# Optimization experiments

Measured on AMD Instinct MI355X. Metric: run time of the kernel, lower is better.

The kernel has to match this reference:

```python
import jax, jax.numpy as jnp
import numpy as np

B, S, HID = 2, 2048, 2048
NH, NKV, HD = 16, 4, 128
EPS = 1e-6
THETA = 10000.0
NEG = jnp.float32(-1e30)


def setup_inputs() -> dict:
    key = jax.random.key(0)
    ks = jax.random.split(key, 7)
    return {
        "hidden_states": jax.random.normal(ks[0], (B, S, HID), jnp.float32) * 0.02,
        "positions": jnp.broadcast_to(jnp.arange(S, dtype=jnp.int32), (B, S)),
        "Wq": jax.random.normal(ks[1], (HID, NH * HD), jnp.float32) * (HID ** -0.5),
        "Wk": jax.random.normal(ks[2], (HID, NKV * HD), jnp.float32) * (HID ** -0.5),
        "Wv": jax.random.normal(ks[3], (HID, NKV * HD), jnp.float32) * (HID ** -0.5),
        "Wc": jax.random.normal(ks[4], (NH * HD, HID), jnp.float32) * ((NH * HD) ** -0.5),
        "q_scale": jax.random.uniform(ks[5], (HD,), jnp.float32),
        "k_scale": jax.random.uniform(ks[6], (HD,), jnp.float32),
    }


def _rmsnorm(x, scale):
    # per-head RMSNorm over head_dim (nnx.RMSNorm semantics)
    return x * jax.lax.rsqrt(jnp.mean(x * x, axis=-1, keepdims=True) + EPS) * scale


def _rope_neox(x, positions):
    # x: [B, S, H, HD]; full rotary_dim == HD, neox style (split halves)
    half = HD // 2
    inv_freq = 1.0 / (THETA ** (jnp.arange(half, dtype=jnp.float32) / half))
    ang = positions[..., None].astype(jnp.float32) * inv_freq  # [B, S, half]
    cos = jnp.cos(ang)[:, :, None, :]
    sin = jnp.sin(ang)[:, :, None, :]
    x1, x2 = jnp.split(x, 2, axis=-1)
    return jnp.concatenate([x1 * cos - x2 * sin, x2 * cos + x1 * sin], axis=-1)


def reference(hidden_states, positions, Wq, Wk, Wv, Wc, q_scale, k_scale):
    q = (hidden_states @ Wq).reshape(B, S, NH, HD)
    k = (hidden_states @ Wk).reshape(B, S, NKV, HD)
    v = (hidden_states @ Wv).reshape(B, S, NKV, HD)
    q = _rmsnorm(q, q_scale)
    k = _rmsnorm(k, k_scale)
    q = _rope_neox(q, positions)
    k = _rope_neox(k, positions)
    # GQA: expand KV heads to query heads
    rep = NH // NKV
    k = jnp.repeat(k, rep, axis=2)
    v = jnp.repeat(v, rep, axis=2)
    scores = jnp.einsum("bqhd,bkhd->bhqk", q, k) * (HD ** -0.5)
    causal = jnp.tril(jnp.ones((S, S), dtype=bool))
    scores = jnp.where(causal, scores, NEG)
    probs = jax.nn.softmax(scores, axis=-1)
    attn = jnp.einsum("bhqk,bkhd->bqhd", probs, v).reshape(B, S, NH * HD)
    return attn @ Wc
```

## Files before the change

### kernel.cpp

```cpp
#include <hip/hip_runtime.h>
#include <stdint.h>

typedef unsigned short u16;
typedef unsigned int u32;
typedef __bf16 bf16x8 __attribute__((ext_vector_type(8)));
typedef float f32x4 __attribute__((ext_vector_type(4)));
typedef u32 u32x4 __attribute__((ext_vector_type(4)));

__device__ __forceinline__ u16 f2bf(float x){
  u32 u = __float_as_uint(x);
  u += 0x7FFFu + ((u >> 16) & 1u);
  return (u16)(u >> 16);
}
__device__ __forceinline__ float bf2f(u16 h){
  return __uint_as_float(((u32)h) << 16);
}
__device__ __forceinline__ u32 cvt_pk_bf16(float lo, float hi){
  u32 r;
  asm("v_cvt_pk_bf16_f32 %0, %1, %2" : "=v"(r) : "v"(lo), "v"(hi));
  return r;
}
__device__ __forceinline__ f32x4 mfma16(bf16x8 a, bf16x8 b, f32x4 c){
  return __builtin_amdgcn_mfma_f32_16x16x32_bf16(a, b, c, 0, 0, 0);
}
__device__ __forceinline__ void gload16(const void* g, const void* l){
  __builtin_amdgcn_global_load_lds(
      (__attribute__((address_space(1))) void*)(uintptr_t)g,
      (__attribute__((address_space(3))) void*)(u32)(uintptr_t)l,
      16, 0, 0);
}

__global__ __launch_bounds__(256) void k_prep(const float* __restrict__ hidden,
    const float* __restrict__ Wq, const float* __restrict__ Wk, const float* __restrict__ Wv,
    const float* __restrict__ Wc, u16* __restrict__ hid_bf, u16* __restrict__ wqkv_t,
    u16* __restrict__ wct, float* __restrict__ ct, float* __restrict__ st){
  __shared__ float tile[32][33];
  int bid = blockIdx.x;
  int t = threadIdx.x;
  if (bid < 8192){
    int i = (bid * 256 + t) * 4;
    float4 v = *(const float4*)(hidden + i);
    ushort4 o;
    o.x = f2bf(v.x); o.y = f2bf(v.y); o.z = f2bf(v.z); o.w = f2bf(v.w);
    *(ushort4*)(hid_bf + i) = o;
    return;
  }
  if (bid < 8192 + 6144){
    int b2 = bid - 8192;
    int nb = (b2 % 96) * 32, kb = (b2 / 96) * 32;
    int tx = t & 31, ty = t >> 5;
    #pragma unroll
    for (int j = 0; j < 4; j++){
      int k = kb + ty + j*8;
      int n = nb + tx;
      float v;
      if (n < 2048)      v = Wq[(size_t)k*2048 + n];
      else if (n < 2560) v = Wk[(size_t)k*512 + (n - 2048)];
      else               v = Wv[(size_t)k*512 + (n - 2560)];
      tile[tx][ty + j*8] = v;
    }
    __syncthreads();
    #pragma unroll
    for (int j = 0; j < 4; j++){
      int n = nb + ty + j*8;
      wqkv_t[(size_t)n*2048 + kb + tx] = f2bf(tile[ty + j*8][tx]);
    }
    return;
  }
  if (bid < 8192 + 6144 + 4096){
    int b3 = bid - 8192 - 6144;
    int nb = (b3 % 64) * 32, kb = (b3 / 64) * 32;
    int tx = t & 31, ty = t >> 5;
    #pragma unroll
    for (int j = 0; j < 4; j++){
      tile[tx][ty + j*8] = Wc[(size_t)(kb + ty + j*8)*2048 + nb + tx];
    }
    __syncthreads();
    #pragma unroll
    for (int j = 0; j < 4; j++){
      wct[(size_t)(nb + ty + j*8)*2048 + kb + tx] = f2bf(tile[ty + j*8][tx]);
    }
    return;
  }
  {
    int b4 = bid - 8192 - 6144 - 4096;
    int idx = b4 * 256 + t;
    int p = idx >> 6, i = idx & 63;
    float freq = powf(10000.0f, -(float)i / 64.0f);
    float ang = (float)p * freq;
    ct[idx] = cosf(ang);
    st[idx] = sinf(ang);
  }
}

__global__ __launch_bounds__(256) void k_gemm_qkv(const u16* __restrict__ A, const u16* __restrict__ Bt,
    u16* __restrict__ qkv, u16* __restrict__ vt, int K){
  __shared__ u16 lds[16384];
  int tid = threadIdx.x;
  int lane = tid & 63, w = tid >> 6;
  int g = lane >> 4, c16 = lane & 15;
  int wr = w >> 1, wc = w & 1;
  int chunk = gridDim.x >> 3;
  int logical = (blockIdx.x & 7) * chunk + (blockIdx.x >> 3);
  int bx = logical % 24, by = logical / 24;
  size_t bm = (size_t)by * 128, bn = (size_t)bx * 128;
  f32x4 zero = {0.f, 0.f, 0.f, 0.f};
  f32x4 acc[4][4];
  #pragma unroll
  for (int i=0;i<4;i++)
    #pragma unroll
    for (int j=0;j<4;j++) acc[i][j] = zero;

  int jj = (w*2)*64 + lane;
  const int nt = K >> 5;
  #pragma unroll
  for (int p = 0; p < 2; p++){
    int j = jj + p*64;
    int r = j >> 2, slot = j & 3;
    gload16(A  + (bm + r)*(size_t)K + slot*8, (const char*)(lds)        + (w*2+p)*1024);
    gload16(Bt + (bn + r)*(size_t)K + slot*8, (const char*)(lds + 8192) + (w*2+p)*1024);
  }
  asm volatile("s_waitcnt vmcnt(0)" ::: "memory");
  __builtin_amdgcn_s_barrier();

  int cur = 0;
  #pragma unroll 1
  for (int t = 0; t < nt; ++t){
    if (t + 1 < nt){
      int k0 = (t + 1) << 5;
      #pragma unroll
      for (int p = 0; p < 2; p++){
        int j = jj + p*64;
        int r = j >> 2, slot = j & 3;
        gload16(A  + (bm + r)*(size_t)K + k0 + slot*8, (const char*)(lds + (cur^1)*4096)        + (w*2+p)*1024);
        gload16(Bt + (bn + r)*(size_t)K + k0 + slot*8, (const char*)(lds + 8192 + (cur^1)*4096) + (w*2+p)*1024);
      }
    }
    const u16* Ac = lds + cur*4096;
    const u16* Bc = lds + 8192 + cur*4096;
    bf16x8 af[4], bfr[4];
    #pragma unroll
    for (int mi=0;mi<4;mi++) af[mi]  = *(const bf16x8*)&Ac[(wr*64 + mi*16 + c16)*32 + g*8];
    #pragma unroll
    for (int ni=0;ni<4;ni++) bfr[ni] = *(const bf16x8*)&Bc[(wc*64 + ni*16 + c16)*32 + g*8];
    #pragma unroll
    for (int mi=0;mi<4;mi++)
      #pragma unroll
      for (int ni=0;ni<4;ni++)
        acc[mi][ni] = mfma16(af[mi], bfr[ni], acc[mi][ni]);
    if (t + 1 < nt){
      asm volatile("s_waitcnt vmcnt(0)" ::: "memory");
      __builtin_amdgcn_s_barrier();
    }
    cur ^= 1;
  }
  if (bx < 20){
    #pragma unroll
    for (int mi=0;mi<4;mi++){
      #pragma unroll
      for (int ni=0;ni<4;ni++){
        #pragma unroll
        for (int r=0;r<4;r++){
          size_t row = bm + wr*64 + mi*16 + g*4 + r;
          size_t col = bn + wc*64 + ni*16 + c16;
          qkv[row * (size_t)3072 + col] = f2bf(acc[mi][ni][r]);
        }
      }
    }
  } else {
    __syncthreads();
    #pragma unroll
    for (int mi=0;mi<4;mi++)
      #pragma unroll
      for (int ni=0;ni<4;ni++)
        #pragma unroll
        for (int r=0;r<4;r++){
          int row = wr*64 + mi*16 + g*4 + r;
          int col = wc*64 + ni*16 + c16;
          lds[col*128 + row] = f2bf(acc[mi][ni][r]);
        }
    __syncthreads();
    int b = (int)(bm >> 11), s0 = (int)(bm & 2047);
    int kvh = bx - 20;
    u16* dst0 = vt + ((size_t)(b*4 + kvh) * 128) * 2048 + s0;
    #pragma unroll
    for (int i = 0; i < 8; i++){
      int ch = i*256 + tid;
      int d = ch >> 4;
      int off = (ch & 15) * 8;
      uint4 vv = *(uint4*)&lds[d*128 + off];
      *(uint4*)(dst0 + (size_t)d*2048 + off) = vv;
    }
  }
}

template<bool OBF>
__global__ __launch_bounds__(256) void k_gemm(const u16* __restrict__ A, const u16* __restrict__ Bt,
                                              void* __restrict__ Cv, int M, int N, int K, int nbx){
  __shared__ u16 As[2][128*32], Bs[2][128*32];
  int tid = threadIdx.x;
  int lane = tid & 63, w = tid >> 6;
  int g = lane >> 4, c16 = lane & 15;
  int wr = w >> 1, wc = w & 1;
  int chunk = gridDim.x >> 3;
  int logical = (blockIdx.x & 7) * chunk + (blockIdx.x >> 3);
  int bx = logical % nbx, by = logical / nbx;
  size_t bm = (size_t)by * 128, bn = (size_t)bx * 128;
  f32x4 zero = {0.f, 0.f, 0.f, 0.f};
  f32x4 acc[4][4];
  #pragma unroll
  for (int i=0;i<4;i++)
    #pragma unroll
    for (int j=0;j<4;j++) acc[i][j] = zero;

  int jj = (w*2)*64 + lane;
  int nt = K >> 5;
  #pragma unroll
  for (int p = 0; p < 2; p++){
    int j = jj + p*64;
    int r = j >> 2, slot = j & 3;
    gload16(A  + (bm + r)*(size_t)K + slot*8, (const char*)As[0] + (w*2+p)*1024);
    gload16(Bt + (bn + r)*(size_t)K + slot*8, (const char*)Bs[0] + (w*2+p)*1024);
  }
  asm volatile("s_waitcnt vmcnt(0)" ::: "memory");
  __builtin_amdgcn_s_barrier();

  int cur = 0;
  #pragma unroll 1
  for (int t = 0; t < nt; ++t){
    if (t + 1 < nt){
      int k0 = (t + 1) << 5;
      #pragma unroll
      for (int p = 0; p < 2; p++){
        int j = jj + p*64;
        int r = j >> 2, slot = j & 3;
        gload16(A  + (bm + r)*(size_t)K + k0 + slot*8, (const char*)As[cur^1] + (w*2+p)*1024);
        gload16(Bt + (bn + r)*(size_t)K + k0 + slot*8, (const char*)Bs[cur^1] + (w*2+p)*1024);
      }
    }
    const u16* Ac = As[cur];
    const u16* Bc = Bs[cur];
    bf16x8 af[4], bfr[4];
    #pragma unroll
    for (int mi=0;mi<4;mi++) af[mi]  = *(const bf16x8*)&Ac[(wr*64 + mi*16 + c16)*32 + g*8];
    #pragma unroll
    for (int ni=0;ni<4;ni++) bfr[ni] = *(const bf16x8*)&Bc[(wc*64 + ni*16 + c16)*32 + g*8];
    #pragma unroll
    for (int mi=0;mi<4;mi++)
      #pragma unroll
      for (int ni=0;ni<4;ni++)
        acc[mi][ni] = mfma16(af[mi], bfr[ni], acc[mi][ni]);
    if (t + 1 < nt){
      asm volatile("s_waitcnt vmcnt(0)" ::: "memory");
      __builtin_amdgcn_s_barrier();
    }
    cur ^= 1;
  }
  #pragma unroll
  for (int mi=0;mi<4;mi++){
    #pragma unroll
    for (int ni=0;ni<4;ni++){
      #pragma unroll
      for (int r=0;r<4;r++){
        size_t row = bm + wr*64 + mi*16 + g*4 + r;
        size_t col = bn + wc*64 + ni*16 + c16;
        if (OBF) ((u16*)Cv)[row * (size_t)N + col] = f2bf(acc[mi][ni][r]);
        else     ((float*)Cv)[row * (size_t)N + col] = acc[mi][ni][r];
      }
    }
  }
}

__global__ __launch_bounds__(256) void k_norm_rope(const u16* __restrict__ qkv, const int* __restrict__ pos,
    const float* __restrict__ qsc, const float* __restrict__ ksc,
    const float* __restrict__ ct, const float* __restrict__ st,
    u16* __restrict__ qo, u16* __restrict__ ko){
  int bs = blockIdx.x;
  int hh = blockIdx.y * 4 + (threadIdx.x >> 6);
  int d = threadIdx.x & 63;
  int b = bs >> 11, s = bs & 2047;
  const u16* row = qkv + (size_t)bs * 3072 + hh * 128;
  u16 r1 = row[d], r2 = row[d + 64];
  float x1 = bf2f(r1), x2 = bf2f(r2);
  float ssq = x1*x1 + x2*x2;
  #pragma unroll
  for (int mm = 1; mm < 64; mm <<= 1) ssq += __shfl_xor(ssq, mm);
  float inv = rsqrtf(ssq * (1.0f/128.0f) + 1e-6f);
  const float* sc = (hh < 16) ? qsc : ksc;
  float y1 = x1 * inv * sc[d];
  float y2 = x2 * inv * sc[d + 64];
  int p = pos[bs];
  float c = ct[p*64 + d], sn = st[p*64 + d];
  float o1 = y1*c - y2*sn;
  float o2 = y2*c + y1*sn;
  if (hh < 16){
    o1 *= 0.1275174528f;
    o2 *= 0.1275174528f;
    size_t o = ((size_t)(b*16 + hh) * 2048 + s) * 128 + d;
    qo[o] = f2bf(o1); qo[o + 64] = f2bf(o2);
  } else {
    size_t o = ((size_t)(b*4 + (hh-16)) * 2048 + s) * 128 + d;
    ko[o] = f2bf(o1); ko[o + 64] = f2bf(o2);
  }
}

__device__ __forceinline__ void stage_kv8(int w, int lane, u16* ksb, u16* vsb,
                                          const u16* kp, const u16* vp, int c0){
  #pragma unroll
  for (int p = 0; p < 2; p++){
    int j = (w*2 + p)*64 + lane;
    int r = j >> 4, slot = j & 15;
    gload16(kp + (size_t)(c0 + r)*128 + ((slot ^ (r & 7)) << 3),
            (const char*)ksb + (w*2 + p)*1024);
  }
  #pragma unroll
  for (int p = 0; p < 2; p++){
    int j = (w*2 + p)*64 + lane;
    int r = j >> 3, slot = j & 7;
    gload16(vp + (size_t)r*2048 + c0 + ((slot ^ (r & 7)) << 3),
            (const char*)vsb + (w*2 + p)*1024);
  }
}

__device__ __forceinline__ void sm_frags(f32x4 (&sacc)[4],
    int qrow, bool diag, int c0, int g, int c16, u32x4* pw){
  if (diag){
    #pragma unroll
    for (int nt = 0; nt < 4; nt++)
      #pragma unroll
      for (int r = 0; r < 4; r++)
        if (c0 + nt*16 + g*4 + r > qrow) sacc[nt][r] = -1e30f;
  }
  #pragma unroll
  for (int nt = 0; nt < 4; nt++)
    #pragma unroll
    for (int r = 0; r < 4; r++)
      sacc[nt][r] = exp2f(sacc[nt][r]);
  u32 pkA[4], pkB[4];
  #pragma unroll
  for (int a = 0; a < 4; a++){
    pkA[a] = cvt_pk_bf16(sacc[a][0], sacc[a][1]);
    pkB[a] = cvt_pk_bf16(sacc[a][2], sacc[a][3]);
  }
  int s0l = (((g*2    ) & 3) << 4) | c16;
  int s1l = (((g*2 + 1) & 3) << 4) | c16;
  bool hi = (g & 2) != 0;
  u32 v0A[4], v0B[4], v1A[4], v1B[4];
  #pragma unroll
  for (int a = 0; a < 4; a++){
    v0A[a] = (u32)__shfl((int)pkA[a], s0l);
    v0B[a] = (u32)__shfl((int)pkB[a], s0l);
    v1A[a] = (u32)__shfl((int)pkA[a], s1l);
    v1B[a] = (u32)__shfl((int)pkB[a], s1l);
  }
  #pragma unroll
  for (int kk2 = 0; kk2 < 2; kk2++){
    pw[kk2].x = hi ? v0A[2*kk2+1] : v0A[2*kk2];
    pw[kk2].y = hi ? v0B[2*kk2+1] : v0B[2*kk2];
    pw[kk2].z = hi ? v1A[2*kk2+1] : v1A[2*kk2];
    pw[kk2].w = hi ? v1B[2*kk2+1] : v1B[2*kk2];
  }
}

__global__ __launch_bounds__(512, 2) void k_attn(const u16* __restrict__ q, const u16* __restrict__ k,
    const u16* __restrict__ vt, u16* __restrict__ attn){
  __shared__ u16 Ks[2][64*128];
  __shared__ u16 Vs[2][128*64];
  int lane = threadIdx.x & 63, w = threadIdx.x >> 6;
  int g = lane >> 4, c16 = lane & 15;
  int wg = w >> 2;
  int wi = w & 3;
  int bid = blockIdx.x;
  int logical = (bid & 7)*64 + (bid >> 3);
  int pi = logical & 15;
  int hb = logical >> 4;
  int h = hb & 15, b = hb >> 4;
  int kvh = h >> 2;
  int qb   = wg ? (31 - pi)*64 : pi*64;
  int tact = wg ? (31 - pi)     : pi;
  int tmax = 31 - pi;
  const u16* qp = q  + ((size_t)(b*16 + h))  * 2048 * 128;
  const u16* kp = k  + ((size_t)(b*4 + kvh)) * 2048 * 128;
  const u16* vp = vt + ((size_t)(b*4 + kvh)) * 128 * 2048;

  int qrow = qb + wi*16 + c16;
  bf16x8 qf[4];
  #pragma unroll
  for (int kk = 0; kk < 4; kk++)
    qf[kk] = *(const bf16x8*)(qp + (size_t)qrow*128 + kk*32 + g*8);
  asm volatile("s_waitcnt vmcnt(0)" ::: "memory");

  u32x4 onesw = {0x3F803F80u, 0x3F803F80u, 0x3F803F80u, 0x3F803F80u};
  bf16x8 ones = __builtin_bit_cast(bf16x8, onesw);

  f32x4 zero = {0.f,0.f,0.f,0.f};
  f32x4 o[8];
  #pragma unroll
  for (int i=0;i<8;i++) o[i] = zero;
  f32x4 l = zero;

  stage_kv8(w, lane, Ks[0], Vs[0], kp, vp, 0);

  for (int t = 0; t <= tmax; t++){
    int c0 = t*64;
    if (t < tmax){
      stage_kv8(w, lane, Ks[(t+1)&1], Vs[(t+1)&1], kp, vp, c0 + 64);
      asm volatile("s_waitcnt vmcnt(4)" ::: "memory");
    } else {
      asm volatile("s_waitcnt vmcnt(0)" ::: "memory");
    }
    __builtin_amdgcn_s_barrier();
    const u16* ksb = Ks[t&1];
    const u16* vsb = Vs[t&1];
    if (t <= tact){
      f32x4 sacc[4];
      #pragma unroll
      for (int i=0;i<4;i++) sacc[i] = zero;
      __builtin_amdgcn_s_setprio(1);
      #pragma unroll
      for (int nt=0;nt<4;nt++){
        #pragma unroll
        for (int kk=0;kk<4;kk++){
          int row = nt*16 + c16;
          bf16x8 kf = *(const bf16x8*)&ksb[row*128 + (((kk*4 + g) ^ (row & 7)) << 3)];
          sacc[nt] = mfma16(kf, qf[kk], sacc[nt]);
        }
      }
      __builtin_amdgcn_s_setprio(0);
      u32x4 pw[2];
      sm_frags(sacc, qrow, t == tact, c0, g, c16, pw);
      __builtin_amdgcn_s_setprio(1);
      #pragma unroll
      for (int kk2 = 0; kk2 < 2; kk2++){
        bf16x8 pf = __builtin_bit_cast(bf16x8, pw[kk2]);
        l = mfma16(pf, ones, l);
        #pragma unroll
        for (int dt = 0; dt < 8; dt++){
          int d = dt*16 + c16;
          bf16x8 vf = *(const bf16x8*)&vsb[d*64 + (((kk2*4 + g) ^ (d & 7)) << 3)];
          o[dt] = mfma16(pf, vf, o[dt]);
        }
      }
      __builtin_amdgcn_s_setprio(0);
    }
    __builtin_amdgcn_sched_barrier(0);
    asm volatile("s_waitcnt lgkmcnt(0)" ::: "memory");
    __builtin_amdgcn_s_barrier();
  }
  float inv[4];
  #pragma unroll
  for (int r = 0; r < 4; r++) inv[r] = 1.0f / l[r];
  #pragma unroll
  for (int dt=0;dt<8;dt++){
    #pragma unroll
    for (int r=0;r<4;r++){
      size_t orow = (size_t)b*2048 + qb + wi*16 + g*4 + r;
      attn[orow*2048 + (size_t)h*128 + dt*16 + c16] = f2bf(o[dt][r] * inv[r]);
    }
  }
}

extern "C" void kernel_launch(void* const* d_in, const int* in_sizes, int n_in,
                              void* d_out, int out_size, void* d_ws, size_t ws_size,
                              hipStream_t stream){
  const float* hidden    = (const float*)d_in[0];
  const int*   positions = (const int*)d_in[1];
  const float* Wq = (const float*)d_in[2];
  const float* Wk = (const float*)d_in[3];
  const float* Wv = (const float*)d_in[4];
  const float* Wc = (const float*)d_in[5];
  const float* qs = (const float*)d_in[6];
  const float* ks = (const float*)d_in[7];
  float* out = (float*)d_out;
  char* ws = (char*)d_ws;
  float* ct      = (float*)(ws + 0);
  float* st      = (float*)(ws + 524288);
  u16*   hid_bf  = (u16*)(ws + 1048576);
  u16*   attn_bf = hid_bf;
  u16*   wqkv_t  = (u16*)(ws + 17825792);
  u16*   wct     = (u16*)(ws + 30408704);
  u16*   qkv_bf  = (u16*)(ws + 38797312);
  u16*   q_bf    = (u16*)(ws + 63963136);
  u16*   k_bf    = (u16*)(ws + 80740352);
  u16*   vt_bf   = (u16*)(ws + 84934656);

  k_prep<<<18944, 256, 0, stream>>>(hidden, Wq, Wk, Wv, Wc, hid_bf, wqkv_t, wct, ct, st);
  k_gemm_qkv<<<768, 256, 0, stream>>>(hid_bf, wqkv_t, qkv_bf, vt_bf, 2048);
  k_norm_rope<<<dim3(4096, 5), 256, 0, stream>>>(qkv_bf, positions, qs, ks, ct, st, q_bf, k_bf);
  k_attn<<<512, 512, 0, stream>>>(q_bf, k_bf, vt_bf, attn_bf);
  k_gemm<false><<<512, 256, 0, stream>>>(attn_bf, wct, (void*)out, 4096, 2048, 2048, 16);
}
```

Before: 206.9 us.

## Permute K row mapping so QK^T output feeds PV MFMA without lane shuffles

Reorders which K rows each lane group loads for the QK^T MFMAs so that the score accumulator layout lines up with the A-operand layout the PV MFMA expects. The 16 cross-lane shuffles and selects per tile are replaced by direct bf16 packing, and the causal mask indices are updated to match the new row order. The K shared-memory swizzle is adjusted so the permuted rows still read without bank conflicts. The risk is a mismatch between the new swizzle, the row mapping and the mask, which would give wrong results rather than a slowdown.

```diff
diff --git a/kernel.cpp b/kernel.cpp
--- a/kernel.cpp
+++ b/kernel.cpp
@@ -310,7 +310,8 @@
   for (int p = 0; p < 2; p++){
     int j = (w*2 + p)*64 + lane;
     int r = j >> 4, slot = j & 15;
-    gload16(kp + (size_t)(c0 + r)*128 + ((slot ^ (r & 7)) << 3),
+    int swzr = (r & 3) | ((r >> 1) & 4);
+    gload16(kp + (size_t)(c0 + r)*128 + ((slot ^ swzr) << 3),
             (const char*)ksb + (w*2 + p)*1024);
   }
   #pragma unroll
@@ -319,46 +320,6 @@
     int r = j >> 3, slot = j & 7;
     gload16(vp + (size_t)r*2048 + c0 + ((slot ^ (r & 7)) << 3),
             (const char*)vsb + (w*2 + p)*1024);
-  }
-}
-
-__device__ __forceinline__ void sm_frags(f32x4 (&sacc)[4],
-    int qrow, bool diag, int c0, int g, int c16, u32x4* pw){
-  if (diag){
-    #pragma unroll
-    for (int nt = 0; nt < 4; nt++)
-      #pragma unroll
-      for (int r = 0; r < 4; r++)
-        if (c0 + nt*16 + g*4 + r > qrow) sacc[nt][r] = -1e30f;
-  }
-  #pragma unroll
-  for (int nt = 0; nt < 4; nt++)
-    #pragma unroll
-    for (int r = 0; r < 4; r++)
-      sacc[nt][r] = exp2f(sacc[nt][r]);
-  u32 pkA[4], pkB[4];
-  #pragma unroll
-  for (int a = 0; a < 4; a++){
-    pkA[a] = cvt_pk_bf16(sacc[a][0], sacc[a][1]);
-    pkB[a] = cvt_pk_bf16(sacc[a][2], sacc[a][3]);
-  }
-  int s0l = (((g*2    ) & 3) << 4) | c16;
-  int s1l = (((g*2 + 1) & 3) << 4) | c16;
-  bool hi = (g & 2) != 0;
-  u32 v0A[4], v0B[4], v1A[4], v1B[4];
-  #pragma unroll
-  for (int a = 0; a < 4; a++){
-    v0A[a] = (u32)__shfl((int)pkA[a], s0l);
-    v0B[a] = (u32)__shfl((int)pkB[a], s0l);
-    v1A[a] = (u32)__shfl((int)pkA[a], s1l);
-    v1B[a] = (u32)__shfl((int)pkB[a], s1l);
-  }
-  #pragma unroll
-  for (int kk2 = 0; kk2 < 2; kk2++){
-    pw[kk2].x = hi ? v0A[2*kk2+1] : v0A[2*kk2];
-    pw[kk2].y = hi ? v0B[2*kk2+1] : v0B[2*kk2];
-    pw[kk2].z = hi ? v1A[2*kk2+1] : v1A[2*kk2];
-    pw[kk2].w = hi ? v1B[2*kk2+1] : v1B[2*kk2];
   }
 }
 
@@ -393,6 +354,9 @@
   u32x4 onesw = {0x3F803F80u, 0x3F803F80u, 0x3F803F80u, 0x3F803F80u};
   bf16x8 ones = __builtin_bit_cast(bf16x8, onesw);
 
+  int rb = 8*(c16 >> 2) + (c16 & 3);
+  int cs = c16 & 7;
+
   f32x4 zero = {0.f,0.f,0.f,0.f};
   f32x4 o[8];
   #pragma unroll
@@ -419,16 +383,35 @@
       __builtin_amdgcn_s_setprio(1);
       #pragma unroll
       for (int nt=0;nt<4;nt++){
+        int R = ((nt >> 1) << 5) + ((nt & 1) << 2) + rb;
         #pragma unroll
         for (int kk=0;kk<4;kk++){
-          int row = nt*16 + c16;
-          bf16x8 kf = *(const bf16x8*)&ksb[row*128 + (((kk*4 + g) ^ (row & 7)) << 3)];
+          bf16x8 kf = *(const bf16x8*)&ksb[R*128 + (((kk*4 + g) ^ cs) << 3)];
           sacc[nt] = mfma16(kf, qf[kk], sacc[nt]);
         }
       }
       __builtin_amdgcn_s_setprio(0);
+      if (t == tact){
+        #pragma unroll
+        for (int nt = 0; nt < 4; nt++)
+          #pragma unroll
+          for (int r = 0; r < 4; r++)
+            if (c0 + ((nt >> 1) << 5) + ((nt & 1) << 2) + 8*g + r > qrow)
+              sacc[nt][r] = -1e30f;
+      }
+      #pragma unroll
+      for (int nt = 0; nt < 4; nt++)
+        #pragma unroll
+        for (int r = 0; r < 4; r++)
+          sacc[nt][r] = exp2f(sacc[nt][r]);
       u32x4 pw[2];
-      sm_frags(sacc, qrow, t == tact, c0, g, c16, pw);
+      #pragma unroll
+      for (int kk2 = 0; kk2 < 2; kk2++){
+        pw[kk2].x = cvt_pk_bf16(sacc[2*kk2][0],   sacc[2*kk2][1]);
+        pw[kk2].y = cvt_pk_bf16(sacc[2*kk2][2],   sacc[2*kk2][3]);
+        pw[kk2].z = cvt_pk_bf16(sacc[2*kk2+1][0], sacc[2*kk2+1][1]);
+        pw[kk2].w = cvt_pk_bf16(sacc[2*kk2+1][2], sacc[2*kk2+1][3]);
+      }
       __builtin_amdgcn_s_setprio(1);
       #pragma unroll
       for (int kk2 = 0; kk2 < 2; kk2++){
```

Measured after the change: 193.5 us, median of 2. 6.5% less time.
